# Kernel tuning notes

Hardware: AMD Instinct MI355X
Metric: run time of the kernel (lower is better)

Reference implementation:

```python
import jax, jax.numpy as jnp
import numpy as np

K = 1024
H = 128

def setup_inputs() -> dict:
    key = jax.random.key(0)
    ks = jax.random.split(key, 11)
    s = lambda fan_in: 1.0 / np.sqrt(fan_in)
    # coord_mlp: Linear(H, H//2) -> GELU -> Linear(H//2, 2)
    cW1 = jax.random.uniform(ks[0], (H, H // 2), minval=-s(H), maxval=s(H))
    cb1 = jax.random.uniform(ks[1], (H // 2,), minval=-s(H), maxval=s(H))
    cW2 = jax.random.uniform(ks[2], (H // 2, 2), minval=-s(H // 2), maxval=s(H // 2))
    cb2 = jax.random.uniform(ks[3], (2,), minval=-s(H // 2), maxval=s(H // 2))
    # edge_mlp: Linear(2H, H) -> GELU -> Linear(H, H//2) -> GELU -> Linear(H//2, 1)
    eW1 = jax.random.uniform(ks[4], (2 * H, H), minval=-s(2 * H), maxval=s(2 * H))
    eb1 = jax.random.uniform(ks[5], (H,), minval=-s(2 * H), maxval=s(2 * H))
    eW2 = jax.random.uniform(ks[6], (H, H // 2), minval=-s(H), maxval=s(H))
    eb2 = jax.random.uniform(ks[7], (H // 2,), minval=-s(H), maxval=s(H))
    eW3 = jax.random.uniform(ks[8], (H // 2, 1), minval=-s(H // 2), maxval=s(H // 2))
    eb3 = jax.random.uniform(ks[9], (1,), minval=-s(H // 2), maxval=s(H // 2))
    z_s = jax.random.normal(ks[10], (K, H), dtype=jnp.float32)
    return {"z_s": z_s, "cW1": cW1, "cb1": cb1, "cW2": cW2, "cb2": cb2,
            "eW1": eW1, "eb1": eb1, "eW2": eW2, "eb2": eb2, "eW3": eW3, "eb3": eb3}

def reference(z_s, cW1, cb1, cW2, cb2, eW1, eb1, eW2, eb2, eW3, eb3):
    gelu = lambda x: jax.nn.gelu(x, approximate=False)  # torch default GELU is exact erf form
    # coords: [k, 2]
    coords_pred = gelu(z_s @ cW1 + cb1) @ cW2 + cb2
    # edge first layer: cat([zi, zj]) @ eW1 == zi @ eW1[:H] + zj @ eW1[H:]
    # (same math as the broadcast-concat, without materializing [k, k, 2H])
    pi = z_s @ eW1[:H]   # [k, H]
    pj = z_s @ eW1[H:]   # [k, H]
    h1 = gelu(pi[:, None, :] + pj[None, :, :] + eb1)   # [k, k, H]
    h2 = gelu(h1 @ eW2 + eb2)                          # [k, k, H//2]
    adj_logits = (h2 @ eW3 + eb3)[..., 0]              # [k, k]
    adj_logits = (adj_logits + adj_logits.T) / 2.0
    return (coords_pred, adj_logits)
```

## Files before the change

kernel.cpp:

```cpp
#include <hip/hip_runtime.h>
#include <hip/hip_fp16.h>


#define KN 1024
#define HN 128

typedef float  floatx4 __attribute__((ext_vector_type(4)));
typedef _Float16 half8v __attribute__((ext_vector_type(8)));

__device__ __forceinline__ float gelu_f(float x) {
    float x2 = x * x;
    float t  = fmaf(x2, -0.1029434f, -2.3022087f);
    float e  = __builtin_amdgcn_exp2f(x * t);
    return x * __builtin_amdgcn_rcpf(e + 1.0f);
}

__device__ __forceinline__ unsigned int gelu2u(unsigned int xu) {
    __half2 x  = __builtin_bit_cast(__half2, xu);
    __half2 x2 = __hmul2(x, x);
    __half2 t  = __hfma2(x2, __float2half2_rn(-0.1029434f),
                             __float2half2_rn(-2.3022087f));
    __half2 e  = h2exp2(__hmul2(x, t));
    __half2 r  = h2rcp(__hadd2(e, __float2half2_rn(1.0f)));
    return __builtin_bit_cast(unsigned int, __hmul2(x, r));
}

__device__ __forceinline__ unsigned int cvt2u(float a, float b) {
    return __builtin_bit_cast(unsigned int, __builtin_amdgcn_cvt_pkrtz(a, b));
}

__device__ __forceinline__ float dotw3(const floatx4* acc, half8v w3f0,
                                       half8v w3f1, float b3) {
    uint4 u0, u1;
    u0.x = gelu2u(cvt2u(acc[0][0], acc[0][1]));
    u0.y = gelu2u(cvt2u(acc[0][2], acc[0][3]));
    u0.z = gelu2u(cvt2u(acc[1][0], acc[1][1]));
    u0.w = gelu2u(cvt2u(acc[1][2], acc[1][3]));
    u1.x = gelu2u(cvt2u(acc[2][0], acc[2][1]));
    u1.y = gelu2u(cvt2u(acc[2][2], acc[2][3]));
    u1.z = gelu2u(cvt2u(acc[3][0], acc[3][1]));
    u1.w = gelu2u(cvt2u(acc[3][2], acc[3][3]));
    half8v h20 = __builtin_bit_cast(half8v, u0);
    half8v h21 = __builtin_bit_cast(half8v, u1);
    floatx4 d = (floatx4){b3, b3, b3, b3};
    d = __builtin_amdgcn_mfma_f32_16x16x32_f16(w3f0, h20, d, 0, 0, 0);
    d = __builtin_amdgcn_mfma_f32_16x16x32_f16(w3f1, h21, d, 0, 0, 0);
    return d[0];
}

__global__ __launch_bounds__(256) void prep_kernel(
    const float* __restrict__ z,   const float* __restrict__ cW1,
    const float* __restrict__ cb1, const float* __restrict__ cW2,
    const float* __restrict__ cb2, const float* __restrict__ eW1,
    const float* __restrict__ eb1, const float* __restrict__ eW2,
    const float* __restrict__ eW3,
    _Float16* __restrict__ pi_h,   _Float16* __restrict__ pj_h,
    _Float16* __restrict__ w2T,    _Float16* __restrict__ w3h,
    float* __restrict__ coords ) {
    __shared__ float z4[4][128];
    __shared__ float c1s[4][64];
    const int tid = threadIdx.x;
    const int r0  = blockIdx.x * 4;

    if (blockIdx.x < 32) {
        int e = blockIdx.x * 256 + tid;
        int d = e >> 7, k = e & 127;
        int R = ((d >> 5) & 1) * 32 + ((d >> 2) & 1) * 16 +
                ((d >> 3) & 3) * 4  + (d & 3);
        w2T[R * 128 + k] = (_Float16)eW2[k * 64 + d];
    }
    if (blockIdx.x == 32 && tid < 64) w3h[tid] = (_Float16)eW3[tid];

#pragma unroll
    for (int s = 0; s < 2; ++s) {
        int e = tid + 256 * s;
        z4[e >> 7][e & 127] = z[r0 * HN + e];
    }
    __syncthreads();

    const int col = tid & 127, which = tid >> 7;
    const float* w = eW1 + which * HN * HN + col;
    float acc4[4] = {0.f, 0.f, 0.f, 0.f};
    for (int k = 0; k < HN; ++k) {
        float wv = w[k * HN];
#pragma unroll
        for (int r = 0; r < 4; ++r) acc4[r] = fmaf(z4[r][k], wv, acc4[r]);
    }
    if (which == 0) {
        float b = eb1[col];
#pragma unroll
        for (int r = 0; r < 4; ++r)
            pi_h[(r0 + r) * HN + col] = (_Float16)(acc4[r] + b);
    } else {
#pragma unroll
        for (int r = 0; r < 4; ++r)
            pj_h[(r0 + r) * HN + col] = (_Float16)acc4[r];
    }

    {
        int row = tid >> 6, mid = tid & 63;
        float a = cb1[mid];
        for (int k = 0; k < HN; ++k) a = fmaf(z4[row][k], cW1[k * 64 + mid], a);
        c1s[row][mid] = gelu_f(a);
    }
    __syncthreads();
    if (tid < 8) {
        int row = tid >> 1, o = tid & 1;
        float a = cb2[o];
#pragma unroll 8
        for (int m = 0; m < 64; ++m) a = fmaf(c1s[row][m], cW2[m * 2 + o], a);
        coords[(r0 + row) * 2 + o] = a;
    }
}

__global__ __launch_bounds__(512, 4) void edge_kernel(
    const _Float16* __restrict__ pi_h, const _Float16* __restrict__ pj_h,
    const _Float16* __restrict__ w2T,  const _Float16* __restrict__ w3h,
    const float* __restrict__ eb2,     const float* __restrict__ eb3,
    float* __restrict__ out_adj) {
    __shared__ __align__(16) unsigned int w2_s[64 * 64];
    const int i0 = blockIdx.y * 32, j0 = blockIdx.x * 32;
    const int tid = threadIdx.x;

    const unsigned int* piu = (const unsigned int*)pi_h;
    const unsigned int* pju = (const unsigned int*)pj_h;
    const unsigned int* w2u = (const unsigned int*)w2T;

#pragma unroll
    for (int s = 0; s < 2; ++s) {
        int e = tid * 4 + 2048 * s;
        int r = e >> 6;
        uint4 v = *reinterpret_cast<const uint4*>(&w2u[e]);
        *reinterpret_cast<uint4*>(&w2_s[e ^ ((r & 7) << 2)]) = v;
    }

    const int lane = tid & 63;
    const int wave = tid >> 6;
    const int lrow = lane & 15;
    const int lhi  = lane >> 4;
    const int lhi4 = lhi << 2;
    const int lhi8 = lhi << 3;
    const int swzW = (lrow & 7) << 2;

    const unsigned int* pjA = &pju[(j0 + lrow) * 64];
    const unsigned int* pjB = &pju[(j0 + 16 + lrow) * 64];
    half8v bA[4], bB[4];
#pragma unroll
    for (int q = 0; q < 4; ++q) {
        const int ko = (q << 4) | lhi4;
        bA[q] = *reinterpret_cast<const half8v*>(&pjA[ko]);
        bB[q] = *reinterpret_cast<const half8v*>(&pjB[ko]);
    }
    const unsigned int* w2base = &w2_s[lrow << 6];

    const half8v w3f0 = *reinterpret_cast<const half8v*>(&w3h[lhi8]);
    const half8v w3f1 = *reinterpret_cast<const half8v*>(&w3h[32 + lhi8]);
    const float4 e0 = *reinterpret_cast<const float4*>(&eb2[lhi8]);
    const float4 e1 = *reinterpret_cast<const float4*>(&eb2[lhi8 + 4]);
    const float4 e2 = *reinterpret_cast<const float4*>(&eb2[32 + lhi8]);
    const float4 e3 = *reinterpret_cast<const float4*>(&eb2[36 + lhi8]);
    const float b3 = eb3[0];
    __syncthreads();

#pragma unroll
    for (int t = 0; t < 4; ++t) {
        const int iL = (wave << 2) + t;
        const unsigned int* pirow = &piu[(size_t)(i0 + iL) * 64];

        floatx4 accA[4], accB[4];
        accA[0] = (floatx4){e0.x, e0.y, e0.z, e0.w};
        accA[1] = (floatx4){e1.x, e1.y, e1.z, e1.w};
        accA[2] = (floatx4){e2.x, e2.y, e2.z, e2.w};
        accA[3] = (floatx4){e3.x, e3.y, e3.z, e3.w};
#pragma unroll
        for (int c = 0; c < 4; ++c) accB[c] = accA[c];

#pragma unroll
        for (int q = 0; q < 4; ++q) {
            const int ko = (q << 4) | lhi4;
            half8v a = *reinterpret_cast<const half8v*>(&pirow[ko]);

            uint4 sA = __builtin_bit_cast(uint4, a + bA[q]);
            uint4 gA;
            gA.x = gelu2u(sA.x); gA.y = gelu2u(sA.y);
            gA.z = gelu2u(sA.z); gA.w = gelu2u(sA.w);
            half8v afA = __builtin_bit_cast(half8v, gA);

            uint4 sB = __builtin_bit_cast(uint4, a + bB[q]);
            uint4 gB;
            gB.x = gelu2u(sB.x); gB.y = gelu2u(sB.y);
            gB.z = gelu2u(sB.z); gB.w = gelu2u(sB.w);
            half8v afB = __builtin_bit_cast(half8v, gB);

            const int kw = ko ^ swzW;
#pragma unroll
            for (int c = 0; c < 4; ++c) {
                half8v bf = *reinterpret_cast<const half8v*>(
                    &w2base[(c << 10) + kw]);
                accA[c] = __builtin_amdgcn_mfma_f32_16x16x32_f16(
                    bf, afA, accA[c], 0, 0, 0);
                accB[c] = __builtin_amdgcn_mfma_f32_16x16x32_f16(
                    bf, afB, accB[c], 0, 0, 0);
            }
        }

        const float dA = dotw3(accA, w3f0, w3f1, b3);
        const float dB = dotw3(accB, w3f0, w3f1, b3);
        if (lhi == 0) {
            float* row = &out_adj[(size_t)(i0 + iL) * KN + j0];
            row[lrow]      = dA;
            row[16 + lrow] = dB;
        }
    }
}

__global__ __launch_bounds__(256) void sym_kernel(float* __restrict__ adj) {
    int idx = blockIdx.x * 256 + threadIdx.x;
    int i = idx >> 10, j = idx & 1023;
    if (j < i) return;
    float a = adj[i * KN + j];
    float b = adj[j * KN + i];
    float m = 0.5f * (a + b);
    adj[i * KN + j] = m;
    adj[j * KN + i] = m;
}

extern "C" void kernel_launch(void* const* d_in, const int* in_sizes, int n_in,
                              void* d_out, int out_size, void* d_ws, size_t ws_size,
                              hipStream_t stream) {
    const float* z   = (const float*)d_in[0];
    const float* cW1 = (const float*)d_in[1];
    const float* cb1 = (const float*)d_in[2];
    const float* cW2 = (const float*)d_in[3];
    const float* cb2 = (const float*)d_in[4];
    const float* eW1 = (const float*)d_in[5];
    const float* eb1 = (const float*)d_in[6];
    const float* eW2 = (const float*)d_in[7];
    const float* eb2 = (const float*)d_in[8];
    const float* eW3 = (const float*)d_in[9];
    const float* eb3 = (const float*)d_in[10];

    float* out = (float*)d_out;
    _Float16* pi_h = (_Float16*)d_ws;
    _Float16* pj_h = pi_h + KN * HN;
    _Float16* w2T  = pj_h + KN * HN;
    _Float16* w3h  = w2T + 64 * HN;

    prep_kernel<<<256, 256, 0, stream>>>(z, cW1, cb1, cW2, cb2, eW1, eb1, eW2,
                                         eW3, pi_h, pj_h, w2T, w3h, out);

    dim3 gridB(32, 32);
    edge_kernel<<<gridB, 512, 0, stream>>>(pi_h, pj_h, w2T, w3h, eb2, eb3,
                                           out + 2048);

    sym_kernel<<<4096, 256, 0, stream>>>(out + 2048);
}
```

Measured before the change: 78.61 us.

## Stage pi/pj tiles in LDS and double edge block height

Each edge block now covers 64 i-rows instead of 32 and halves the grid. The pi and pj rows are staged into swizzled shared memory, and the per-row pi and pj fragments are read from LDS instead of global memory. The aim is to amortize the W2 LDS load over more rows and to cut global reads. The cost is more LDS per block (about 40KB), which may lower occupancy, plus scalar 4-byte staging loads replacing the earlier uint4 loads.

```diff
diff --git a/kernel.cpp b/kernel.cpp
--- a/kernel.cpp
+++ b/kernel.cpp
@@ -118,8 +118,10 @@
     const _Float16* __restrict__ w2T,  const _Float16* __restrict__ w3h,
     const float* __restrict__ eb2,     const float* __restrict__ eb3,
     float* __restrict__ out_adj) {
+    __shared__ __align__(16) unsigned int pi_s[64 * 64];
+    __shared__ __align__(16) unsigned int pj_s[32 * 64];
     __shared__ __align__(16) unsigned int w2_s[64 * 64];
-    const int i0 = blockIdx.y * 32, j0 = blockIdx.x * 32;
+    const int i0 = blockIdx.y * 64, j0 = blockIdx.x * 32;
     const int tid = threadIdx.x;
 
     const unsigned int* piu = (const unsigned int*)pi_h;
@@ -127,11 +129,22 @@
     const unsigned int* w2u = (const unsigned int*)w2T;
 
 #pragma unroll
-    for (int s = 0; s < 2; ++s) {
-        int e = tid * 4 + 2048 * s;
+    for (int s = 0; s < 8; ++s) {
+        int e = tid + 512 * s;
         int r = e >> 6;
-        uint4 v = *reinterpret_cast<const uint4*>(&w2u[e]);
-        *reinterpret_cast<uint4*>(&w2_s[e ^ ((r & 7) << 2)]) = v;
+        pi_s[e ^ ((r & 7) << 2)] = piu[(i0 + r) * 64 + (e & 63)];
+    }
+#pragma unroll
+    for (int s = 0; s < 4; ++s) {
+        int e = tid + 512 * s;
+        int r = e >> 6;
+        pj_s[e ^ ((r & 7) << 2)] = pju[(j0 + r) * 64 + (e & 63)];
+    }
+#pragma unroll
+    for (int s = 0; s < 8; ++s) {
+        int e = tid + 512 * s;
+        int r = e >> 6;
+        w2_s[e ^ ((r & 7) << 2)] = w2u[e];
     }
 
     const int lane = tid & 63;
@@ -140,18 +153,7 @@
     const int lhi  = lane >> 4;
     const int lhi4 = lhi << 2;
     const int lhi8 = lhi << 3;
-    const int swzW = (lrow & 7) << 2;
-
-    const unsigned int* pjA = &pju[(j0 + lrow) * 64];
-    const unsigned int* pjB = &pju[(j0 + 16 + lrow) * 64];
-    half8v bA[4], bB[4];
-#pragma unroll
-    for (int q = 0; q < 4; ++q) {
-        const int ko = (q << 4) | lhi4;
-        bA[q] = *reinterpret_cast<const half8v*>(&pjA[ko]);
-        bB[q] = *reinterpret_cast<const half8v*>(&pjB[ko]);
-    }
-    const unsigned int* w2base = &w2_s[lrow << 6];
+    const int swzJ = (lrow & 7) << 2;
 
     const half8v w3f0 = *reinterpret_cast<const half8v*>(&w3h[lhi8]);
     const half8v w3f1 = *reinterpret_cast<const half8v*>(&w3h[32 + lhi8]);
@@ -162,10 +164,22 @@
     const float b3 = eb3[0];
     __syncthreads();
 
-#pragma unroll
-    for (int t = 0; t < 4; ++t) {
-        const int iL = (wave << 2) + t;
-        const unsigned int* pirow = &piu[(size_t)(i0 + iL) * 64];
+    const unsigned int* pjA = &pj_s[lrow << 6];
+    const unsigned int* pjB = &pj_s[(16 + lrow) << 6];
+    half8v bA[4], bB[4];
+#pragma unroll
+    for (int q = 0; q < 4; ++q) {
+        const int ko = ((q << 4) | lhi4) ^ swzJ;
+        bA[q] = *reinterpret_cast<const half8v*>(&pjA[ko]);
+        bB[q] = *reinterpret_cast<const half8v*>(&pjB[ko]);
+    }
+    const unsigned int* w2base = &w2_s[lrow << 6];
+
+#pragma unroll
+    for (int t = 0; t < 8; ++t) {
+        const int iL = (wave << 3) + t;
+        const unsigned int* pirow = &pi_s[iL << 6];
+        const int swzI = t << 2;
 
         floatx4 accA[4], accB[4];
         accA[0] = (floatx4){e0.x, e0.y, e0.z, e0.w};
@@ -178,7 +192,7 @@
 #pragma unroll
         for (int q = 0; q < 4; ++q) {
             const int ko = (q << 4) | lhi4;
-            half8v a = *reinterpret_cast<const half8v*>(&pirow[ko]);
+            half8v a = *reinterpret_cast<const half8v*>(&pirow[ko ^ swzI]);
 
             uint4 sA = __builtin_bit_cast(uint4, a + bA[q]);
             uint4 gA;
@@ -192,7 +206,7 @@
             gB.z = gelu2u(sB.z); gB.w = gelu2u(sB.w);
             half8v afB = __builtin_bit_cast(half8v, gB);
 
-            const int kw = ko ^ swzW;
+            const int kw = ko ^ swzJ;
 #pragma unroll
             for (int c = 0; c < 4; ++c) {
                 half8v bf = *reinterpret_cast<const half8v*>(
@@ -249,7 +263,7 @@
     prep_kernel<<<256, 256, 0, stream>>>(z, cW1, cb1, cW2, cb2, eW1, eb1, eW2,
                                          eW3, pi_h, pj_h, w2T, w3h, out);
 
-    dim3 gridB(32, 32);
+    dim3 gridB(32, 16);
     edge_kernel<<<gridB, 512, 0, stream>>>(pi_h, pj_h, w2T, w3h, eb2, eb3,
                                            out + 2048);
 
```

After: 75.58 us (median of 2 runs). 1.04x faster.
